# Kernel optimization log

Hardware: AMD Instinct MI355X
Metric: run time of the kernel (lower is better)

Reference implementation:

```python
import jax, jax.numpy as jnp
import numpy as np

A = 81          # agents / zones (9x9 grid)
DMAX = 5        # max neighborhood size (self + 4-neighbors)
NGLOB = 48      # global obs block width
HID = 128
B = 16384
LN_EPS = 1e-12  # tf.contrib.layers.layer_norm epsilon
BN_EPS = 1e-3   # tf.contrib.layers.batch_norm epsilon
NEG = -1e30


def _grid_adjacency():
    side = 9
    idx = np.zeros((A, DMAX), np.int32)
    mask = np.zeros((A, DMAX), bool)
    for i in range(A):
        r, c = divmod(i, side)
        nb = [i]
        for dr, dc in ((-1, 0), (1, 0), (0, -1), (0, 1)):
            rr, cc = r + dr, c + dc
            if 0 <= rr < side and 0 <= cc < side:
                nb.append(rr * side + cc)
        idx[i, :len(nb)] = nb
        mask[i, :len(nb)] = True
    return jnp.asarray(idx), jnp.asarray(mask)


def setup_inputs() -> dict:
    key = jax.random.key(0)
    ks = jax.random.split(key, 8)
    neigh_idx, neigh_mask = _grid_adjacency()
    in_dim = 2 * DMAX + NGLOB  # padded local obs width (58)
    s = 0.05
    return {
        "obs": jax.random.normal(ks[0], (B, 210), jnp.float32),
        "neigh_idx": neigh_idx,
        "neigh_mask": neigh_mask,
        "W1": jax.random.normal(ks[1], (A, in_dim, HID), jnp.float32) * s,
        "b1": jnp.zeros((A, HID), jnp.float32),
        "ln1_g": jnp.ones((A, HID), jnp.float32),
        "ln1_b": jnp.zeros((A, HID), jnp.float32),
        "bn1_b": jnp.zeros((A, HID), jnp.float32),
        "W2": jax.random.normal(ks[2], (A, HID, HID), jnp.float32) * s,
        "b2": jnp.zeros((A, HID), jnp.float32),
        "ln2_g": jnp.ones((A, HID), jnp.float32),
        "ln2_b": jnp.zeros((A, HID), jnp.float32),
        "bn2_b": jnp.zeros((A, HID), jnp.float32),
        "Wout": jax.random.normal(ks[3], (A, HID, DMAX), jnp.float32) * s,
        "bout": jnp.zeros((A, DMAX), jnp.float32),
    }


def _layer_norm(x, g, b):
    mu = jnp.mean(x, axis=-1, keepdims=True)
    var = jnp.mean(jnp.square(x - mu), axis=-1, keepdims=True)
    return (x - mu) * jax.lax.rsqrt(var + LN_EPS) * g[:, None, :] + b[:, None, :]


def _batch_norm(x, beta):
    # training-mode batch norm over the batch axis (axis=1), center only (scale=False)
    mu = jnp.mean(x, axis=1, keepdims=True)
    var = jnp.mean(jnp.square(x - mu), axis=1, keepdims=True)
    return (x - mu) * jax.lax.rsqrt(var + BN_EPS) + beta[:, None, :]


def reference(obs, neigh_idx, neigh_mask, W1, b1, ln1_g, ln1_b, bn1_b,
              W2, b2, ln2_g, ln2_b, bn2_b, Wout, bout):
    m = neigh_mask[:, None, :].astype(obs.dtype)          # [A,1,DMAX]
    g1 = obs[:, NGLOB + neigh_idx].transpose(1, 0, 2)      # [A,B,DMAX] zone block 1
    g2 = obs[:, NGLOB + 81 + neigh_idx].transpose(1, 0, 2)  # [A,B,DMAX] zone block 2
    glob = jnp.broadcast_to(obs[None, :, :NGLOB], (A, obs.shape[0], NGLOB))
    x = jnp.concatenate([g1 * m, g2 * m, glob], axis=-1)   # [A,B,58] (padded slots zeroed)

    h = jnp.einsum('abi,aio->abo', x, W1) + b1[:, None, :]
    h = jax.nn.relu(_batch_norm(_layer_norm(h, ln1_g, ln1_b), bn1_b))
    h = jnp.einsum('abi,aio->abo', h, W2) + b2[:, None, :]
    h = jax.nn.relu(_batch_norm(_layer_norm(h, ln2_g, ln2_b), bn2_b))

    logits = jnp.einsum('abi,aid->abd', h, Wout) + bout[:, None, :]  # [A,B,DMAX]
    logits = jnp.where(neigh_mask[:, None, :], logits, NEG)
    p = jax.nn.softmax(logits, axis=-1) * m                # masked softmax over valid neighbors

    oh = jax.nn.one_hot(neigh_idx, A, dtype=p.dtype)       # [A,DMAX,81] scatter map
    out = jnp.einsum('abd,adn->abn', p, oh)                # scatter into fixed 81-vector
    return out.transpose(1, 0, 2)                          # [B,A,81]
```

## Files before the change

### kernel.cpp

```cpp
#include <hip/hip_runtime.h>
#include <stdint.h>
#include <stddef.h>

#define N_AG 81

typedef __bf16 bf16x8 __attribute__((ext_vector_type(8)));
typedef float f32x4 __attribute__((ext_vector_type(4)));
typedef uint32_t u32v4 __attribute__((ext_vector_type(4)));
typedef uint32_t u32v2 __attribute__((ext_vector_type(2)));

#define PB 0
#define PG 128
#define PBT 256

#define SWZ(row, off) ((uint32_t)(off) ^ (((uint32_t)(row) & 7u) << 4))

__device__ __forceinline__ unsigned short b2u(__bf16 h) {
  return __builtin_bit_cast(unsigned short, h);
}

__device__ __forceinline__ f32x4 f4z() { f32x4 v; v[0]=0.f; v[1]=0.f; v[2]=0.f; v[3]=0.f; return v; }

__device__ __forceinline__ bf16x8 ld_frag(const uint8_t* p) {
  u32v4 v = *(const u32v4*)p;
  return __builtin_bit_cast(bf16x8, v);
}

__device__ __forceinline__ f32x4 mfma16(bf16x8 a, bf16x8 b, f32x4 c) {
  return __builtin_amdgcn_mfma_f32_16x16x32_bf16(a, b, c, 0, 0, 0);
}

__device__ __forceinline__ uint8_t* yslot(float* out, int b, int a) {
  size_t base = (size_t)b * 26244 + (size_t)a * 324;
  uint32_t pad = (uint32_t)(64 - (base & 63)) & 63u;
  return (uint8_t*)out + base + pad;
}

__device__ __forceinline__ float wave16_sum(float v) {
  v += __builtin_bit_cast(float, __builtin_amdgcn_update_dpp(0, __builtin_bit_cast(int, v), 0xB1, 0xF, 0xF, true));
  v += __builtin_bit_cast(float, __builtin_amdgcn_update_dpp(0, __builtin_bit_cast(int, v), 0x4E, 0xF, 0xF, true));
  v += __builtin_bit_cast(float, __builtin_amdgcn_update_dpp(0, __builtin_bit_cast(int, v), 0x141, 0xF, 0xF, true));
  v += __builtin_bit_cast(float, __builtin_amdgcn_update_dpp(0, __builtin_bit_cast(int, v), 0x140, 0xF, 0xF, true));
  return v;
}

__device__ __forceinline__ bf16x8 mk_frag(const unsigned short (&us)[8]) {
  u32v4 pk;
  pk[0] = (uint32_t)us[0] | ((uint32_t)us[1] << 16);
  pk[1] = (uint32_t)us[2] | ((uint32_t)us[3] << 16);
  pk[2] = (uint32_t)us[4] | ((uint32_t)us[5] << 16);
  pk[3] = (uint32_t)us[6] | ((uint32_t)us[7] << 16);
  return __builtin_bit_cast(bf16x8, pk);
}

__device__ __forceinline__ bf16x8 bn_frag(u32v4 yv, const f32x4 (&cf)[4]) {
  bf16x8 r;
  #pragma unroll
  for (int j = 0; j < 8; ++j) {
    uint32_t us = (j & 1) ? (yv[j >> 1] >> 16) : (yv[j >> 1] & 0xffffu);
    float f = __builtin_bit_cast(float, us << 16);
    float h = fmaf(f, cf[j >> 1][(j & 1) * 2], cf[j >> 1][(j & 1) * 2 + 1]);
    r[j] = (__bf16)fmaxf(h, 0.f);
  }
  return r;
}

__device__ __forceinline__ void bias_ln(f32x4 (&acc)[8][2], const float* s_par, int g) {
  #pragma unroll
  for (int nf = 0; nf < 2; ++nf) {
    float s = 0.f, qs = 0.f;
    #pragma unroll
    for (int mf = 0; mf < 8; ++mf) {
      #pragma unroll
      for (int rg = 0; rg < 4; ++rg) {
        float tv = acc[mf][nf][rg] + s_par[PB + 16 * mf + 4 * g + rg];
        acc[mf][nf][rg] = tv;
        s += tv;
        qs = fmaf(tv, tv, qs);
      }
    }
    s += __shfl_xor(s, 16);  s += __shfl_xor(s, 32);
    qs += __shfl_xor(qs, 16); qs += __shfl_xor(qs, 32);
    float mu = s * (1.f / 128.f);
    float var = qs * (1.f / 128.f) - mu * mu;
    float rstd = rsqrtf(var + 1e-12f);
    #pragma unroll
    for (int mf = 0; mf < 8; ++mf) {
      #pragma unroll
      for (int rg = 0; rg < 4; ++rg) {
        int o = 16 * mf + 4 * g + rg;
        acc[mf][nf][rg] = (acc[mf][nf][rg] - mu) * rstd * s_par[PG + o] + s_par[PBT + o];
      }
    }
  }
}

__device__ __forceinline__ void stats_lds(const f32x4 (&acc)[8][2],
                                          float (&s_red)[2][4][128],
                                          int wv, int g, int q) {
  #pragma unroll
  for (int mf = 0; mf < 8; ++mf) {
    #pragma unroll
    for (int rg = 0; rg < 4; ++rg) {
      float a0v = acc[mf][0][rg], a1v = acc[mf][1][rg];
      float s = a0v + a1v;
      float qq = fmaf(a0v, a0v, a1v * a1v);
      s = wave16_sum(s);
      qq = wave16_sum(qq);
      if (q == 0) {
        int o = 16 * mf + 4 * g + rg;
        s_red[0][wv][o] += s;
        s_red[1][wv][o] += qq;
      }
    }
  }
}

__device__ __forceinline__ void pack_lds(const f32x4 (&acc)[8][2], uint8_t* s_y,
                                         int wv, int g, int q) {
  #pragma unroll
  for (int nf = 0; nf < 2; ++nf) {
    uint32_t row = 32 * wv + 16 * nf + q;
    #pragma unroll
    for (int mf = 0; mf < 8; ++mf) {
      u32v2 pk;
      pk[0] = (uint32_t)b2u((__bf16)acc[mf][nf][0]) | ((uint32_t)b2u((__bf16)acc[mf][nf][1]) << 16);
      pk[1] = (uint32_t)b2u((__bf16)acc[mf][nf][2]) | ((uint32_t)b2u((__bf16)acc[mf][nf][3]) << 16);
      *(u32v2*)(s_y + row * 256 + SWZ(row, 32 * mf + 8 * g)) = pk;
    }
  }
}

__device__ __forceinline__ void burst_out(const uint8_t* s_y, float* out, int tile, int a, int t) {
  const int row = t >> 1, half = t & 1;
  uint8_t* sp = yslot(out, tile * 128 + row, a) + half * 128;
  #pragma unroll
  for (int j = 0; j < 8; ++j) {
    u32v4 v = *(const u32v4*)(s_y + row * 256 + SWZ(row, half * 128 + 16 * j));
    *(u32v4*)(sp + 16 * j) = v;
  }
}

__device__ __forceinline__ void burst_in(uint8_t* s_y, float* out, int tile, int a, int t) {
  const int row = t >> 1, half = t & 1;
  const uint8_t* sp = yslot(out, tile * 128 + row, a) + half * 128;
  #pragma unroll
  for (int j = 0; j < 8; ++j) {
    u32v4 v = *(const u32v4*)(sp + 16 * j);
    *(u32v4*)(s_y + row * 256 + SWZ(row, half * 128 + 16 * j)) = v;
  }
}

__global__ void prep_w1(const float* __restrict__ W1, uint8_t* __restrict__ w1img) {
  const int a = blockIdx.x, t = threadIdx.x;
  for (int i = t; i < 128 * 64; i += 256) {
    int o = i & 127, kk = i >> 7;
    float v;
    if (kk < 48)      v = W1[((size_t)a * 58 + (10 + kk)) * 128 + o];
    else if (kk < 58) v = W1[((size_t)a * 58 + (kk - 48)) * 128 + o];
    else              v = 0.f;
    uint32_t cb = 2u * kk;
    uint32_t phys = o * 128 + (((cb & ~15u) ^ (((uint32_t)o & 7u) << 4)) | (cb & 15u));
    *(unsigned short*)(w1img + (size_t)a * 16384 + phys) = b2u((__bf16)v);
  }
}

__global__ void prep_w2wo(const float* __restrict__ W2, const float* __restrict__ Wout,
                          uint8_t* __restrict__ w2img, uint8_t* __restrict__ woimg) {
  const int a = blockIdx.x, t = threadIdx.x;
  for (int i = t; i < 128 * 128; i += 256) {
    int o = i & 127, kk = i >> 7;
    float v = W2[((size_t)a * 128 + kk) * 128 + o];
    uint32_t cb = 2u * kk;
    uint32_t phys = o * 256 + (((cb & ~15u) ^ (((uint32_t)o & 7u) << 4)) | (cb & 15u));
    *(unsigned short*)(w2img + (size_t)a * 32768 + phys) = b2u((__bf16)v);
  }
  for (int i = t; i < 16 * 128; i += 256) {
    int k = i & 127, d = i >> 7;
    float v = (d < 5) ? Wout[((size_t)a * 128 + k) * 5 + d] : 0.f;
    uint32_t cb = 2u * k;
    uint32_t phys = d * 256 + (((cb & ~15u) ^ (((uint32_t)d & 7u) << 4)) | (cb & 15u));
    *(unsigned short*)(woimg + (size_t)a * 4096 + phys) = b2u((__bf16)v);
  }
}

__global__ void prep_obs(const float* __restrict__ obs, uint8_t* __restrict__ globimg) {
  const int row = blockIdx.x * 256 + threadIdx.x;
  if (row >= 16384) return;
  const float* orow = obs + (size_t)row * 210;
  uint8_t* dst = globimg + (size_t)row * 96;
  #pragma unroll
  for (int c = 0; c < 6; ++c) {
    u32v4 pk;
    #pragma unroll
    for (int e = 0; e < 4; ++e) {
      pk[e] = (uint32_t)b2u((__bf16)orow[8 * c + 2 * e]) |
              ((uint32_t)b2u((__bf16)orow[8 * c + 2 * e + 1]) << 16);
    }
    *(u32v4*)(dst + 16 * c) = pk;
  }
}

__global__ void prep_zimgT(const float* __restrict__ obs, unsigned short* __restrict__ zimgT) {
  __shared__ unsigned short lt[128][164];
  const int t = threadIdx.x;
  const int b0 = blockIdx.x * 128;
  for (int i = t; i < 128 * 162; i += 256) {
    int br = i / 162, n = i - 162 * br;
    lt[br][n] = b2u((__bf16)obs[(size_t)(b0 + br) * 210 + 48 + n]);
  }
  __syncthreads();
  for (int i = t; i < 162 * 128; i += 256) {
    int n = i >> 7, br = i & 127;
    zimgT[(size_t)n * 16384 + b0 + br] = lt[br][n];
  }
}

__global__ void reduce_bn(const float* __restrict__ S, const float* __restrict__ Q,
                          const float* __restrict__ beta, float2* __restrict__ bn) {
  const int a = blockIdx.x, k = threadIdx.x;
  float mu = S[a * 128 + k] * (1.f / 16384.f);
  float var = Q[a * 128 + k] * (1.f / 16384.f) - mu * mu;
  float rs = rsqrtf(var + 1e-3f);
  bn[a * 128 + k] = make_float2(rs, beta[a * 128 + k] - mu * rs);
}

__launch_bounds__(256, 2)
__global__ void pass1_kernel(const int* __restrict__ nidx,
                             const float* __restrict__ b1, const float* __restrict__ ln1g,
                             const float* __restrict__ ln1b,
                             const uint8_t* __restrict__ w1img,
                             const uint8_t* __restrict__ globimg,
                             const unsigned short* __restrict__ zimgT,
                             float* __restrict__ statS, float* __restrict__ statQ,
                             float* __restrict__ out) {
  __shared__ __align__(16) uint8_t s_w1[16384];
  __shared__ __align__(16) uint8_t s_y[32768];
  __shared__ float s_par[384];
  __shared__ float s_red[2][4][128];

  const int t = threadIdx.x;
  const int wv = t >> 6, l = t & 63, g = l >> 4, q = l & 15;
  const int a = blockIdx.x >> 5;
  const int sub = blockIdx.x & 31;

  const int r9 = a / 9, c9 = a - 9 * r9;
  const int deg = 1 + (r9 > 0) + (r9 < 8) + (c9 > 0) + (c9 < 8);
  int nid[5];
  #pragma unroll
  for (int d = 0; d < 5; ++d) nid[d] = __builtin_amdgcn_readfirstlane(nidx[a * 5 + d]);

  const uint8_t* w1src = w1img + (size_t)a * 16384;
  #pragma unroll
  for (int i = 0; i < 4; ++i) ((u32v4*)s_w1)[t + 256 * i] = ((const u32v4*)w1src)[t + 256 * i];
  if (t < 128) {
    s_par[PB + t] = b1[a * 128 + t];
    s_par[PG + t] = ln1g[a * 128 + t];
    s_par[PBT + t] = ln1b[a * 128 + t];
  }
  #pragma unroll
  for (int i = 0; i < 4; ++i) ((float*)s_red)[t + 256 * i] = 0.f;
  __syncthreads();

  for (int tt = 0; tt < 4; ++tt) {
    const int tile = sub * 4 + tt;

    bf16x8 bfr[2][2];
    #pragma unroll
    for (int ks = 0; ks < 2; ++ks) {
      #pragma unroll
      for (int nf = 0; nf < 2; ++nf) {
        const int brow = tile * 128 + 32 * wv + 16 * nf + q;
        if (ks == 1 && g >= 2) {
          unsigned short us[8];
          if (g == 2) {
            #pragma unroll
            for (int e = 0; e < 5; ++e)
              us[e] = (e < deg) ? zimgT[(size_t)nid[e] * 16384 + brow] : (unsigned short)0;
            #pragma unroll
            for (int e = 0; e < 3; ++e)
              us[5 + e] = (e < deg) ? zimgT[(size_t)(81 + nid[e]) * 16384 + brow] : (unsigned short)0;
          } else {
            us[0] = (3 < deg) ? zimgT[(size_t)(81 + nid[3]) * 16384 + brow] : (unsigned short)0;
            us[1] = (4 < deg) ? zimgT[(size_t)(81 + nid[4]) * 16384 + brow] : (unsigned short)0;
            #pragma unroll
            for (int e = 2; e < 8; ++e) us[e] = 0;
          }
          bfr[ks][nf] = mk_frag(us);
        } else {
          bfr[ks][nf] = *(const bf16x8*)(globimg + (size_t)brow * 96 + (32 * ks + 8 * g) * 2);
        }
      }
    }

    f32x4 acc[8][2];
    #pragma unroll
    for (int mf = 0; mf < 8; ++mf) { acc[mf][0] = f4z(); acc[mf][1] = f4z(); }
    #pragma unroll
    for (int ks = 0; ks < 2; ++ks) {
      #pragma unroll
      for (int mf = 0; mf < 8; ++mf) {
        uint32_t r = 16 * mf + q;
        uint32_t cb = ((uint32_t)(64 * ks + 16 * g)) ^ ((r & 7u) << 4);
        bf16x8 af = ld_frag(s_w1 + r * 128 + cb);
        acc[mf][0] = mfma16(af, bfr[ks][0], acc[mf][0]);
        acc[mf][1] = mfma16(af, bfr[ks][1], acc[mf][1]);
      }
    }

    bias_ln(acc, s_par, g);
    stats_lds(acc, s_red, wv, g, q);
    pack_lds(acc, s_y, wv, g, q);
    __syncthreads();
    burst_out(s_y, out, tile, a, t);
    __syncthreads();
  }

  if (t < 128) {
    float S = s_red[0][0][t] + s_red[0][1][t] + s_red[0][2][t] + s_red[0][3][t];
    float Q = s_red[1][0][t] + s_red[1][1][t] + s_red[1][2][t] + s_red[1][3][t];
    atomicAdd(statS + a * 128 + t, S);
    atomicAdd(statQ + a * 128 + t, Q);
  }
}

__launch_bounds__(256, 2)
__global__ void pass2_kernel(const float* __restrict__ b2, const float* __restrict__ ln2g,
                             const float* __restrict__ ln2b,
                             const uint8_t* __restrict__ w2img,
                             const float2* __restrict__ bn1,
                             float* __restrict__ statS, float* __restrict__ statQ,
                             float* __restrict__ out) {
  __shared__ __align__(16) uint8_t s_w2[32768];
  __shared__ __align__(16) uint8_t s_y[32768];
  __shared__ float s_par[384];
  __shared__ __align__(16) float2 s_bnc[128];
  __shared__ float s_red[2][4][128];

  const int t = threadIdx.x;
  const int wv = t >> 6, l = t & 63, g = l >> 4, q = l & 15;
  const int a = blockIdx.x >> 5;
  const int sub = blockIdx.x & 31;

  const uint8_t* w2src = w2img + (size_t)a * 32768;
  #pragma unroll
  for (int i = 0; i < 8; ++i) ((u32v4*)s_w2)[t + 256 * i] = ((const u32v4*)w2src)[t + 256 * i];
  if (t < 128) {
    s_par[PB + t] = b2[a * 128 + t];
    s_par[PG + t] = ln2g[a * 128 + t];
    s_par[PBT + t] = ln2b[a * 128 + t];
    s_bnc[t] = bn1[a * 128 + t];
  }
  #pragma unroll
  for (int i = 0; i < 4; ++i) ((float*)s_red)[t + 256 * i] = 0.f;
  __syncthreads();

  for (int tt = 0; tt < 4; ++tt) {
    const int tile = sub * 4 + tt;

    burst_in(s_y, out, tile, a, t);
    __syncthreads();

    f32x4 acc[8][2];
    #pragma unroll
    for (int mf = 0; mf < 8; ++mf) { acc[mf][0] = f4z(); acc[mf][1] = f4z(); }

    #pragma unroll
    for (int ks2 = 0; ks2 < 4; ++ks2) {
      const int k0 = 32 * ks2 + 8 * g;
      f32x4 cf[4];
      #pragma unroll
      for (int i = 0; i < 4; ++i)
        cf[i] = *(const f32x4*)((const uint8_t*)s_bnc + k0 * 8 + 16 * i);
      bf16x8 bfr[2];
      #pragma unroll
      for (int nf = 0; nf < 2; ++nf) {
        uint32_t row = 32 * wv + 16 * nf + q;
        u32v4 yv = *(const u32v4*)(s_y + row * 256 + SWZ(row, 64 * ks2 + 16 * g));
        bfr[nf] = bn_frag(yv, cf);
      }
      #pragma unroll
      for (int mf = 0; mf < 8; ++mf) {
        uint32_t r = 16 * mf + q;
        uint32_t cb = ((uint32_t)(64 * ks2 + 16 * g)) ^ ((r & 7u) << 4);
        bf16x8 af = ld_frag(s_w2 + r * 256 + cb);
        acc[mf][0] = mfma16(af, bfr[0], acc[mf][0]);
        acc[mf][1] = mfma16(af, bfr[1], acc[mf][1]);
      }
    }

    bias_ln(acc, s_par, g);
    stats_lds(acc, s_red, wv, g, q);
    __syncthreads();
    pack_lds(acc, s_y, wv, g, q);
    __syncthreads();
    burst_out(s_y, out, tile, a, t);
    __syncthreads();
  }

  if (t < 128) {
    float S = s_red[0][0][t] + s_red[0][1][t] + s_red[0][2][t] + s_red[0][3][t];
    float Q = s_red[1][0][t] + s_red[1][1][t] + s_red[1][2][t] + s_red[1][3][t];
    atomicAdd(statS + a * 128 + t, S);
    atomicAdd(statQ + a * 128 + t, Q);
  }
}

__launch_bounds__(256, 3)
__global__ void pass3_kernel(const int* __restrict__ nidx, const float* __restrict__ boutp,
                             const uint8_t* __restrict__ woimg,
                             const float2* __restrict__ bn2,
                             float* __restrict__ out) {
  __shared__ __align__(16) uint8_t s_buf[43008];
  __shared__ __align__(16) uint8_t s_wo[4096];
  __shared__ __align__(16) float2 s_bnc[128];
  __shared__ float s_bout[16];

  uint8_t* s_y = s_buf;
  float* s_out = (float*)s_buf;

  const int t = threadIdx.x;
  const int wv = t >> 6, l = t & 63, g = l >> 4, q = l & 15;
  const int a = blockIdx.x >> 5;
  const int sub = blockIdx.x & 31;

  const int r9 = a / 9, c9 = a - 9 * r9;
  const int deg = 1 + (r9 > 0) + (r9 < 8) + (c9 > 0) + (c9 < 8);
  int nid[5];
  #pragma unroll
  for (int d = 0; d < 5; ++d) nid[d] = __builtin_amdgcn_readfirstlane(nidx[a * 5 + d]);

  ((u32v4*)s_wo)[t] = ((const u32v4*)(woimg + (size_t)a * 4096))[t];
  if (t < 128) s_bnc[t] = bn2[a * 128 + t];
  if (t < 16) s_bout[t] = (t < 5) ? boutp[a * 5 + t] : 0.f;
  __syncthreads();

  bf16x8 afr[4];
  #pragma unroll
  for (int ks2 = 0; ks2 < 4; ++ks2) {
    uint32_t cb = ((uint32_t)(64 * ks2 + 16 * g)) ^ (((uint32_t)q & 7u) << 4);
    afr[ks2] = ld_frag(s_wo + q * 256 + cb);
  }

  for (int tt = 0; tt < 4; ++tt) {
    const int tile = sub * 4 + tt;

    burst_in(s_y, out, tile, a, t);
    __syncthreads();

    f32x4 accd[2];
    accd[0] = f4z(); accd[1] = f4z();

    #pragma unroll
    for (int ks2 = 0; ks2 < 4; ++ks2) {
      const int k0 = 32 * ks2 + 8 * g;
      f32x4 cf[4];
      #pragma unroll
      for (int i = 0; i < 4; ++i)
        cf[i] = *(const f32x4*)((const uint8_t*)s_bnc + k0 * 8 + 16 * i);
      #pragma unroll
      for (int nf = 0; nf < 2; ++nf) {
        uint32_t row = 32 * wv + 16 * nf + q;
        u32v4 yv = *(const u32v4*)(s_y + row * 256 + SWZ(row, 64 * ks2 + 16 * g));
        accd[nf] = mfma16(afr[ks2], bn_frag(yv, cf), accd[nf]);
      }
    }

    #pragma unroll
    for (int nf = 0; nf < 2; ++nf) {
      #pragma unroll
      for (int rg = 0; rg < 4; ++rg) accd[nf][rg] += s_bout[4 * g + rg];
    }
    float d4[2];
    d4[0] = __shfl_xor(accd[0][0], 16);
    d4[1] = __shfl_xor(accd[1][0], 16);

    float p[2][5];
    #pragma unroll
    for (int nf = 0; nf < 2; ++nf) {
      float v[5] = {accd[nf][0], accd[nf][1], accd[nf][2], accd[nf][3], d4[nf]};
      float mx = v[0];
      #pragma unroll
      for (int d = 1; d < 5; ++d)
        if (d < deg) mx = fmaxf(mx, v[d]);
      float den = 0.f;
      #pragma unroll
      for (int d = 0; d < 5; ++d) {
        float e = (d < deg) ? __expf(v[d] - mx) : 0.f;
        p[nf][d] = e;
        den += e;
      }
      float inv = 1.f / den;
      #pragma unroll
      for (int d = 0; d < 5; ++d) p[nf][d] *= inv;
    }

    float p5[5];
    #pragma unroll
    for (int d = 0; d < 5; ++d) {
      float pr = __shfl_xor(p[1][d], 32);
      p5[d] = (g == 0) ? p[0][d] : pr;
    }

    __syncthreads();
    #pragma unroll
    for (int i = 0; i < 11; ++i) {
      int idx = t + 256 * i;
      if (idx < 2688) {
        u32v4 z; z[0] = 0u; z[1] = 0u; z[2] = 0u; z[3] = 0u;
        ((u32v4*)s_out)[idx] = z;
      }
    }
    __syncthreads();
    if (g == 0 || g == 2) {
      const int row = 32 * wv + ((g == 2) ? 16 : 0) + q;
      #pragma unroll
      for (int d = 0; d < 5; ++d)
        if (d < deg) s_out[row * 84 + nid[d]] = p5[d];
    }
    __syncthreads();
    const size_t obase = (size_t)(tile * 128) * 6561 + (size_t)a * 81;
    for (int i = t; i < 128 * 81; i += 256) {
      int r = i / 81;
      int n = i - r * 81;
      out[obase + (size_t)r * 6561 + n] = s_out[r * 84 + n];
    }
    __syncthreads();
  }
}

extern "C" void kernel_launch(void* const* d_in, const int* in_sizes, int n_in,
                              void* d_out, int out_size, void* d_ws, size_t ws_size,
                              hipStream_t stream) {
  (void)in_sizes; (void)n_in; (void)out_size; (void)ws_size;
  const float* obs = (const float*)d_in[0];
  const int* nidx = (const int*)d_in[1];
  const float* W1 = (const float*)d_in[3];
  const float* b1 = (const float*)d_in[4];
  const float* ln1g = (const float*)d_in[5];
  const float* ln1b = (const float*)d_in[6];
  const float* bnb1 = (const float*)d_in[7];
  const float* W2 = (const float*)d_in[8];
  const float* b2 = (const float*)d_in[9];
  const float* ln2g = (const float*)d_in[10];
  const float* ln2b = (const float*)d_in[11];
  const float* bnb2 = (const float*)d_in[12];
  const float* Wout = (const float*)d_in[13];
  const float* bout = (const float*)d_in[14];
  float* out = (float*)d_out;
  uint8_t* ws = (uint8_t*)d_ws;

  uint8_t* w1img   = ws;
  uint8_t* globimg = ws + 1327104;
  uint8_t* regionA = ws + 2899968;
  unsigned short* zimgT = (unsigned short*)regionA;
  uint8_t* w2img = regionA;
  uint8_t* woimg = regionA + 2654208;
  float* statS = (float*)(ws + 8208384);
  float* statQ = (float*)(ws + 8249856);
  float2* bn1 = (float2*)(ws + 8291328);
  float2* bn2 = (float2*)(ws + 8374272);

  prep_w1<<<N_AG, 256, 0, stream>>>(W1, w1img);
  prep_obs<<<64, 256, 0, stream>>>(obs, globimg);
  prep_zimgT<<<128, 256, 0, stream>>>(obs, zimgT);
  hipMemsetAsync(statS, 0, 2 * 41472, stream);

  pass1_kernel<<<N_AG * 32, 256, 0, stream>>>(nidx, b1, ln1g, ln1b, w1img, globimg, zimgT,
                                              statS, statQ, out);
  reduce_bn<<<N_AG, 128, 0, stream>>>(statS, statQ, bnb1, bn1);

  prep_w2wo<<<N_AG, 256, 0, stream>>>(W2, Wout, w2img, woimg);
  hipMemsetAsync(statS, 0, 2 * 41472, stream);

  pass2_kernel<<<N_AG * 32, 256, 0, stream>>>(b2, ln2g, ln2b, w2img, bn1,
                                              statS, statQ, out);
  reduce_bn<<<N_AG, 128, 0, stream>>>(statS, statQ, bnb2, bn2);

  pass3_kernel<<<N_AG * 32, 256, 0, stream>>>(nidx, bout, woimg, bn2, out);
}
```

Measured before the change: 777.8 us.

## Recompute hidden layers per pass instead of spilling activations through output buffer

Instead of writing the layer-1 and layer-2 activations to the output buffer as scratch and reading them back in later passes, each pass now recomputes earlier layers from obs: pass2 redoes GEMM1 and pass3 redoes GEMM1 and GEMM2. The zone-transpose prep kernel is removed, and zone features are gathered directly from obs. Weights are read from global memory instead of being staged in LDS, which lowers LDS use and allows higher occupancy bounds. This trades a large amount of intermediate global traffic for extra MFMA work and scattered obs reads.

```diff
diff --git a/kernel.cpp b/kernel.cpp
--- a/kernel.cpp
+++ b/kernel.cpp
@@ -13,7 +13,7 @@
 #define PG 128
 #define PBT 256
 
-#define SWZ(row, off) ((uint32_t)(off) ^ (((uint32_t)(row) & 7u) << 4))
+#define SWZ(row, off) ((uint32_t)(off) ^ (((uint32_t)(row) & 15u) << 4))
 
 __device__ __forceinline__ unsigned short b2u(__bf16 h) {
   return __builtin_bit_cast(unsigned short, h);
@@ -28,12 +28,6 @@
 
 __device__ __forceinline__ f32x4 mfma16(bf16x8 a, bf16x8 b, f32x4 c) {
   return __builtin_amdgcn_mfma_f32_16x16x32_bf16(a, b, c, 0, 0, 0);
-}
-
-__device__ __forceinline__ uint8_t* yslot(float* out, int b, int a) {
-  size_t base = (size_t)b * 26244 + (size_t)a * 324;
-  uint32_t pad = (uint32_t)(64 - (base & 63)) & 63u;
-  return (uint8_t*)out + base + pad;
 }
 
 __device__ __forceinline__ float wave16_sum(float v) {
@@ -53,16 +47,79 @@
   return __builtin_bit_cast(bf16x8, pk);
 }
 
-__device__ __forceinline__ bf16x8 bn_frag(u32v4 yv, const f32x4 (&cf)[4]) {
-  bf16x8 r;
-  #pragma unroll
-  for (int j = 0; j < 8; ++j) {
-    uint32_t us = (j & 1) ? (yv[j >> 1] >> 16) : (yv[j >> 1] & 0xffffu);
-    float f = __builtin_bit_cast(float, us << 16);
-    float h = fmaf(f, cf[j >> 1][(j & 1) * 2], cf[j >> 1][(j & 1) * 2 + 1]);
-    r[j] = (__bf16)fmaxf(h, 0.f);
-  }
-  return r;
+__device__ __forceinline__ bf16x8 zone_frag(const float* orow, const int (&nid)[5],
+                                            int deg, int g) {
+  unsigned short us[8];
+  if (g == 2) {
+    #pragma unroll
+    for (int e = 0; e < 8; ++e) {
+      float v;
+      if (e < 5) v = (e < deg) ? orow[48 + nid[e]] : 0.f;
+      else       v = ((e - 5) < deg) ? orow[129 + nid[e - 5]] : 0.f;
+      us[e] = b2u((__bf16)v);
+    }
+  } else {
+    us[0] = (3 < deg) ? b2u((__bf16)orow[129 + nid[3]]) : (unsigned short)0;
+    us[1] = (4 < deg) ? b2u((__bf16)orow[129 + nid[4]]) : (unsigned short)0;
+    #pragma unroll
+    for (int e = 2; e < 8; ++e) us[e] = 0;
+  }
+  return mk_frag(us);
+}
+
+__device__ __forceinline__ void build_xfrags(bf16x8 (&bfr)[2][2],
+                                             const uint8_t* __restrict__ globimg,
+                                             const float* __restrict__ obs,
+                                             int tile, int wv, int g, int q,
+                                             const int (&nid)[5], int deg) {
+  #pragma unroll
+  for (int ks = 0; ks < 2; ++ks) {
+    #pragma unroll
+    for (int nf = 0; nf < 2; ++nf) {
+      const int brow = tile * 128 + 32 * wv + 16 * nf + q;
+      if (ks == 1 && g >= 2) {
+        bfr[ks][nf] = zone_frag(obs + (size_t)brow * 210, nid, deg, g);
+      } else {
+        bfr[ks][nf] = *(const bf16x8*)(globimg + (size_t)brow * 96 + (32 * ks + 8 * g) * 2);
+      }
+    }
+  }
+}
+
+__device__ __forceinline__ void gemm1(f32x4 (&acc)[8][2], const bf16x8 (&bfr)[2][2],
+                                      const uint8_t* __restrict__ w1a, int g, int q) {
+  #pragma unroll
+  for (int ks = 0; ks < 2; ++ks) {
+    #pragma unroll
+    for (int mf = 0; mf < 8; ++mf) {
+      uint32_t r = 16 * mf + q;
+      uint32_t cb = ((uint32_t)(64 * ks + 16 * g)) ^ ((r & 7u) << 4);
+      bf16x8 af = ld_frag(w1a + r * 128 + cb);
+      acc[mf][0] = mfma16(af, bfr[ks][0], acc[mf][0]);
+      acc[mf][1] = mfma16(af, bfr[ks][1], acc[mf][1]);
+    }
+  }
+}
+
+__device__ __forceinline__ void gemm2(f32x4 (&acc)[8][2], const uint8_t* __restrict__ s_y,
+                                      const uint8_t* __restrict__ w2a, int wv, int g, int q) {
+  #pragma unroll
+  for (int ks2 = 0; ks2 < 4; ++ks2) {
+    bf16x8 bfr2[2];
+    #pragma unroll
+    for (int nf = 0; nf < 2; ++nf) {
+      uint32_t row = 32 * wv + 16 * nf + q;
+      bfr2[nf] = ld_frag(s_y + row * 256 + SWZ(row, 64 * ks2 + 16 * g));
+    }
+    #pragma unroll
+    for (int mf = 0; mf < 8; ++mf) {
+      uint32_t r = 16 * mf + q;
+      uint32_t cb = ((uint32_t)(64 * ks2 + 16 * g)) ^ ((r & 7u) << 4);
+      bf16x8 af = ld_frag(w2a + r * 256 + cb);
+      acc[mf][0] = mfma16(af, bfr2[0], acc[mf][0]);
+      acc[mf][1] = mfma16(af, bfr2[1], acc[mf][1]);
+    }
+  }
 }
 
 __device__ __forceinline__ void bias_ln(f32x4 (&acc)[8][2], const float* s_par, int g) {
@@ -116,38 +173,26 @@
   }
 }
 
-__device__ __forceinline__ void pack_lds(const f32x4 (&acc)[8][2], uint8_t* s_y,
-                                         int wv, int g, int q) {
+__device__ __forceinline__ void pack_h(const f32x4 (&acc)[8][2], const float2* s_bnc,
+                                       uint8_t* s_y, int wv, int g, int q) {
   #pragma unroll
   for (int nf = 0; nf < 2; ++nf) {
     uint32_t row = 32 * wv + 16 * nf + q;
     #pragma unroll
     for (int mf = 0; mf < 8; ++mf) {
+      unsigned short us[4];
+      #pragma unroll
+      for (int rg = 0; rg < 4; ++rg) {
+        int o = 16 * mf + 4 * g + rg;
+        float2 c = s_bnc[o];
+        float h = fmaf(acc[mf][nf][rg], c.x, c.y);
+        us[rg] = b2u((__bf16)fmaxf(h, 0.f));
+      }
       u32v2 pk;
-      pk[0] = (uint32_t)b2u((__bf16)acc[mf][nf][0]) | ((uint32_t)b2u((__bf16)acc[mf][nf][1]) << 16);
-      pk[1] = (uint32_t)b2u((__bf16)acc[mf][nf][2]) | ((uint32_t)b2u((__bf16)acc[mf][nf][3]) << 16);
+      pk[0] = (uint32_t)us[0] | ((uint32_t)us[1] << 16);
+      pk[1] = (uint32_t)us[2] | ((uint32_t)us[3] << 16);
       *(u32v2*)(s_y + row * 256 + SWZ(row, 32 * mf + 8 * g)) = pk;
     }
-  }
-}
-
-__device__ __forceinline__ void burst_out(const uint8_t* s_y, float* out, int tile, int a, int t) {
-  const int row = t >> 1, half = t & 1;
-  uint8_t* sp = yslot(out, tile * 128 + row, a) + half * 128;
-  #pragma unroll
-  for (int j = 0; j < 8; ++j) {
-    u32v4 v = *(const u32v4*)(s_y + row * 256 + SWZ(row, half * 128 + 16 * j));
-    *(u32v4*)(sp + 16 * j) = v;
-  }
-}
-
-__device__ __forceinline__ void burst_in(uint8_t* s_y, float* out, int tile, int a, int t) {
-  const int row = t >> 1, half = t & 1;
-  const uint8_t* sp = yslot(out, tile * 128 + row, a) + half * 128;
-  #pragma unroll
-  for (int j = 0; j < 8; ++j) {
-    u32v4 v = *(const u32v4*)(sp + 16 * j);
-    *(u32v4*)(s_y + row * 256 + SWZ(row, half * 128 + 16 * j)) = v;
   }
 }
 
@@ -201,21 +246,6 @@
   }
 }
 
-__global__ void prep_zimgT(const float* __restrict__ obs, unsigned short* __restrict__ zimgT) {
-  __shared__ unsigned short lt[128][164];
-  const int t = threadIdx.x;
-  const int b0 = blockIdx.x * 128;
-  for (int i = t; i < 128 * 162; i += 256) {
-    int br = i / 162, n = i - 162 * br;
-    lt[br][n] = b2u((__bf16)obs[(size_t)(b0 + br) * 210 + 48 + n]);
-  }
-  __syncthreads();
-  for (int i = t; i < 162 * 128; i += 256) {
-    int n = i >> 7, br = i & 127;
-    zimgT[(size_t)n * 16384 + b0 + br] = lt[br][n];
-  }
-}
-
 __global__ void reduce_bn(const float* __restrict__ S, const float* __restrict__ Q,
                           const float* __restrict__ beta, float2* __restrict__ bn) {
   const int a = blockIdx.x, k = threadIdx.x;
@@ -225,18 +255,14 @@
   bn[a * 128 + k] = make_float2(rs, beta[a * 128 + k] - mu * rs);
 }
 
-__launch_bounds__(256, 2)
-__global__ void pass1_kernel(const int* __restrict__ nidx,
+__launch_bounds__(256, 4)
+__global__ void pass1_kernel(const float* __restrict__ obs, const int* __restrict__ nidx,
                              const float* __restrict__ b1, const float* __restrict__ ln1g,
                              const float* __restrict__ ln1b,
                              const uint8_t* __restrict__ w1img,
                              const uint8_t* __restrict__ globimg,
-                             const unsigned short* __restrict__ zimgT,
-                             float* __restrict__ statS, float* __restrict__ statQ,
-                             float* __restrict__ out) {
-  __shared__ __align__(16) uint8_t s_w1[16384];
-  __shared__ __align__(16) uint8_t s_y[32768];
-  __shared__ float s_par[384];
+                             float* __restrict__ statS, float* __restrict__ statQ) {
+  __shared__ float s_parA[384];
   __shared__ float s_red[2][4][128];
 
   const int t = threadIdx.x;
@@ -250,72 +276,30 @@
   #pragma unroll
   for (int d = 0; d < 5; ++d) nid[d] = __builtin_amdgcn_readfirstlane(nidx[a * 5 + d]);
 
-  const uint8_t* w1src = w1img + (size_t)a * 16384;
-  #pragma unroll
-  for (int i = 0; i < 4; ++i) ((u32v4*)s_w1)[t + 256 * i] = ((const u32v4*)w1src)[t + 256 * i];
   if (t < 128) {
-    s_par[PB + t] = b1[a * 128 + t];
-    s_par[PG + t] = ln1g[a * 128 + t];
-    s_par[PBT + t] = ln1b[a * 128 + t];
+    s_parA[PB + t] = b1[a * 128 + t];
+    s_parA[PG + t] = ln1g[a * 128 + t];
+    s_parA[PBT + t] = ln1b[a * 128 + t];
   }
   #pragma unroll
   for (int i = 0; i < 4; ++i) ((float*)s_red)[t + 256 * i] = 0.f;
   __syncthreads();
 
+  const uint8_t* w1a = w1img + (size_t)a * 16384;
+
   for (int tt = 0; tt < 4; ++tt) {
     const int tile = sub * 4 + tt;
-
     bf16x8 bfr[2][2];
-    #pragma unroll
-    for (int ks = 0; ks < 2; ++ks) {
-      #pragma unroll
-      for (int nf = 0; nf < 2; ++nf) {
-        const int brow = tile * 128 + 32 * wv + 16 * nf + q;
-        if (ks == 1 && g >= 2) {
-          unsigned short us[8];
-          if (g == 2) {
-            #pragma unroll
-            for (int e = 0; e < 5; ++e)
-              us[e] = (e < deg) ? zimgT[(size_t)nid[e] * 16384 + brow] : (unsigned short)0;
-            #pragma unroll
-            for (int e = 0; e < 3; ++e)
-              us[5 + e] = (e < deg) ? zimgT[(size_t)(81 + nid[e]) * 16384 + brow] : (unsigned short)0;
-          } else {
-            us[0] = (3 < deg) ? zimgT[(size_t)(81 + nid[3]) * 16384 + brow] : (unsigned short)0;
-            us[1] = (4 < deg) ? zimgT[(size_t)(81 + nid[4]) * 16384 + brow] : (unsigned short)0;
-            #pragma unroll
-            for (int e = 2; e < 8; ++e) us[e] = 0;
-          }
-          bfr[ks][nf] = mk_frag(us);
-        } else {
-          bfr[ks][nf] = *(const bf16x8*)(globimg + (size_t)brow * 96 + (32 * ks + 8 * g) * 2);
-        }
-      }
-    }
-
+    build_xfrags(bfr, globimg, obs, tile, wv, g, q, nid, deg);
     f32x4 acc[8][2];
     #pragma unroll
     for (int mf = 0; mf < 8; ++mf) { acc[mf][0] = f4z(); acc[mf][1] = f4z(); }
-    #pragma unroll
-    for (int ks = 0; ks < 2; ++ks) {
-      #pragma unroll
-      for (int mf = 0; mf < 8; ++mf) {
-        uint32_t r = 16 * mf + q;
-        uint32_t cb = ((uint32_t)(64 * ks + 16 * g)) ^ ((r & 7u) << 4);
-        bf16x8 af = ld_frag(s_w1 + r * 128 + cb);
-        acc[mf][0] = mfma16(af, bfr[ks][0], acc[mf][0]);
-        acc[mf][1] = mfma16(af, bfr[ks][1], acc[mf][1]);
-      }
-    }
-
-    bias_ln(acc, s_par, g);
+    gemm1(acc, bfr, w1a, g, q);
+    bias_ln(acc, s_parA, g);
     stats_lds(acc, s_red, wv, g, q);
-    pack_lds(acc, s_y, wv, g, q);
-    __syncthreads();
-    burst_out(s_y, out, tile, a, t);
-    __syncthreads();
-  }
-
+  }
+
+  __syncthreads();
   if (t < 128) {
     float S = s_red[0][0][t] + s_red[0][1][t] + s_red[0][2][t] + s_red[0][3][t];
     float Q = s_red[1][0][t] + s_red[1][1][t] + s_red[1][2][t] + s_red[1][3][t];
@@ -324,17 +308,21 @@
   }
 }
 
-__launch_bounds__(256, 2)
-__global__ void pass2_kernel(const float* __restrict__ b2, const float* __restrict__ ln2g,
+__launch_bounds__(256, 3)
+__global__ void pass2_kernel(const float* __restrict__ obs, const int* __restrict__ nidx,
+                             const float* __restrict__ b1, const float* __restrict__ ln1g,
+                             const float* __restrict__ ln1b,
+                             const float* __restrict__ b2, const float* __restrict__ ln2g,
                              const float* __restrict__ ln2b,
+                             const uint8_t* __restrict__ w1img,
                              const uint8_t* __restrict__ w2img,
+                             const uint8_t* __restrict__ globimg,
                              const float2* __restrict__ bn1,
-                             float* __restrict__ statS, float* __restrict__ statQ,
-                             float* __restrict__ out) {
-  __shared__ __align__(16) uint8_t s_w2[32768];
+                             float* __restrict__ statS, float* __restrict__ statQ) {
   __shared__ __align__(16) uint8_t s_y[32768];
-  __shared__ float s_par[384];
-  __shared__ __align__(16) float2 s_bnc[128];
+  __shared__ float s_parA[384];
+  __shared__ float s_parB[384];
+  __shared__ __align__(16) float2 s_bnc1[128];
   __shared__ float s_red[2][4][128];
 
   const int t = threadIdx.x;
@@ -342,62 +330,51 @@
   const int a = blockIdx.x >> 5;
   const int sub = blockIdx.x & 31;
 
-  const uint8_t* w2src = w2img + (size_t)a * 32768;
-  #pragma unroll
-  for (int i = 0; i < 8; ++i) ((u32v4*)s_w2)[t + 256 * i] = ((const u32v4*)w2src)[t + 256 * i];
+  const int r9 = a / 9, c9 = a - 9 * r9;
+  const int deg = 1 + (r9 > 0) + (r9 < 8) + (c9 > 0) + (c9 < 8);
+  int nid[5];
+  #pragma unroll
+  for (int d = 0; d < 5; ++d) nid[d] = __builtin_amdgcn_readfirstlane(nidx[a * 5 + d]);
+
   if (t < 128) {
-    s_par[PB + t] = b2[a * 128 + t];
-    s_par[PG + t] = ln2g[a * 128 + t];
-    s_par[PBT + t] = ln2b[a * 128 + t];
-    s_bnc[t] = bn1[a * 128 + t];
+    s_parA[PB + t] = b1[a * 128 + t];
+    s_parA[PG + t] = ln1g[a * 128 + t];
+    s_parA[PBT + t] = ln1b[a * 128 + t];
+    s_parB[PB + t] = b2[a * 128 + t];
+    s_parB[PG + t] = ln2g[a * 128 + t];
+    s_parB[PBT + t] = ln2b[a * 128 + t];
+    s_bnc1[t] = bn1[a * 128 + t];
   }
   #pragma unroll
   for (int i = 0; i < 4; ++i) ((float*)s_red)[t + 256 * i] = 0.f;
   __syncthreads();
 
+  const uint8_t* w1a = w1img + (size_t)a * 16384;
+  const uint8_t* w2a = w2img + (size_t)a * 32768;
+
   for (int tt = 0; tt < 4; ++tt) {
     const int tile = sub * 4 + tt;
-
-    burst_in(s_y, out, tile, a, t);
-    __syncthreads();
-
-    f32x4 acc[8][2];
-    #pragma unroll
-    for (int mf = 0; mf < 8; ++mf) { acc[mf][0] = f4z(); acc[mf][1] = f4z(); }
-
-    #pragma unroll
-    for (int ks2 = 0; ks2 < 4; ++ks2) {
-      const int k0 = 32 * ks2 + 8 * g;
-      f32x4 cf[4];
-      #pragma unroll
-      for (int i = 0; i < 4; ++i)
-        cf[i] = *(const f32x4*)((const uint8_t*)s_bnc + k0 * 8 + 16 * i);
-      bf16x8 bfr[2];
-      #pragma unroll
-      for (int nf = 0; nf < 2; ++nf) {
-        uint32_t row = 32 * wv + 16 * nf + q;
-        u32v4 yv = *(const u32v4*)(s_y + row * 256 + SWZ(row, 64 * ks2 + 16 * g));
-        bfr[nf] = bn_frag(yv, cf);
-      }
-      #pragma unroll
-      for (int mf = 0; mf < 8; ++mf) {
-        uint32_t r = 16 * mf + q;
-        uint32_t cb = ((uint32_t)(64 * ks2 + 16 * g)) ^ ((r & 7u) << 4);
-        bf16x8 af = ld_frag(s_w2 + r * 256 + cb);
-        acc[mf][0] = mfma16(af, bfr[0], acc[mf][0]);
-        acc[mf][1] = mfma16(af, bfr[1], acc[mf][1]);
-      }
-    }
-
-    bias_ln(acc, s_par, g);
-    stats_lds(acc, s_red, wv, g, q);
-    __syncthreads();
-    pack_lds(acc, s_y, wv, g, q);
-    __syncthreads();
-    burst_out(s_y, out, tile, a, t);
-    __syncthreads();
-  }
-
+    bf16x8 bfr[2][2];
+    build_xfrags(bfr, globimg, obs, tile, wv, g, q, nid, deg);
+    f32x4 acc1[8][2];
+    #pragma unroll
+    for (int mf = 0; mf < 8; ++mf) { acc1[mf][0] = f4z(); acc1[mf][1] = f4z(); }
+    gemm1(acc1, bfr, w1a, g, q);
+    bias_ln(acc1, s_parA, g);
+
+    __syncthreads();
+    pack_h(acc1, s_bnc1, s_y, wv, g, q);
+    __syncthreads();
+
+    f32x4 acc2[8][2];
+    #pragma unroll
+    for (int mf = 0; mf < 8; ++mf) { acc2[mf][0] = f4z(); acc2[mf][1] = f4z(); }
+    gemm2(acc2, s_y, w2a, wv, g, q);
+    bias_ln(acc2, s_parB, g);
+    stats_lds(acc2, s_red, wv, g, q);
+  }
+
+  __syncthreads();
   if (t < 128) {
     float S = s_red[0][0][t] + s_red[0][1][t] + s_red[0][2][t] + s_red[0][3][t];
     float Q = s_red[1][0][t] + s_red[1][1][t] + s_red[1][2][t] + s_red[1][3][t];
@@ -407,13 +384,23 @@
 }
 
 __launch_bounds__(256, 3)
-__global__ void pass3_kernel(const int* __restrict__ nidx, const float* __restrict__ boutp,
+__global__ void pass3_kernel(const float* __restrict__ obs, const int* __restrict__ nidx,
+                             const float* __restrict__ b1, const float* __restrict__ ln1g,
+                             const float* __restrict__ ln1b,
+                             const float* __restrict__ b2, const float* __restrict__ ln2g,
+                             const float* __restrict__ ln2b,
+                             const float* __restrict__ boutp,
+                             const uint8_t* __restrict__ w1img,
+                             const uint8_t* __restrict__ w2img,
                              const uint8_t* __restrict__ woimg,
-                             const float2* __restrict__ bn2,
+                             const uint8_t* __restrict__ globimg,
+                             const float2* __restrict__ bn1, const float2* __restrict__ bn2,
                              float* __restrict__ out) {
   __shared__ __align__(16) uint8_t s_buf[43008];
-  __shared__ __align__(16) uint8_t s_wo[4096];
-  __shared__ __align__(16) float2 s_bnc[128];
+  __shared__ float s_parA[384];
+  __shared__ float s_parB[384];
+  __shared__ __align__(16) float2 s_bnc1[128];
+  __shared__ __align__(16) float2 s_bnc2[128];
   __shared__ float s_bout[16];
 
   uint8_t* s_y = s_buf;
@@ -430,39 +417,64 @@
   #pragma unroll
   for (int d = 0; d < 5; ++d) nid[d] = __builtin_amdgcn_readfirstlane(nidx[a * 5 + d]);
 
-  ((u32v4*)s_wo)[t] = ((const u32v4*)(woimg + (size_t)a * 4096))[t];
-  if (t < 128) s_bnc[t] = bn2[a * 128 + t];
+  if (t < 128) {
+    s_parA[PB + t] = b1[a * 128 + t];
+    s_parA[PG + t] = ln1g[a * 128 + t];
+    s_parA[PBT + t] = ln1b[a * 128 + t];
+    s_parB[PB + t] = b2[a * 128 + t];
+    s_parB[PG + t] = ln2g[a * 128 + t];
+    s_parB[PBT + t] = ln2b[a * 128 + t];
+    s_bnc1[t] = bn1[a * 128 + t];
+    s_bnc2[t] = bn2[a * 128 + t];
+  }
   if (t < 16) s_bout[t] = (t < 5) ? boutp[a * 5 + t] : 0.f;
   __syncthreads();
 
+  const uint8_t* w1a = w1img + (size_t)a * 16384;
+  const uint8_t* w2a = w2img + (size_t)a * 32768;
+  const uint8_t* woa = woimg + (size_t)a * 4096;
+
   bf16x8 afr[4];
   #pragma unroll
   for (int ks2 = 0; ks2 < 4; ++ks2) {
     uint32_t cb = ((uint32_t)(64 * ks2 + 16 * g)) ^ (((uint32_t)q & 7u) << 4);
-    afr[ks2] = ld_frag(s_wo + q * 256 + cb);
+    afr[ks2] = ld_frag(woa + q * 256 + cb);
   }
 
   for (int tt = 0; tt < 4; ++tt) {
     const int tile = sub * 4 + tt;
 
-    burst_in(s_y, out, tile, a, t);
+    bf16x8 bfr[2][2];
+    build_xfrags(bfr, globimg, obs, tile, wv, g, q, nid, deg);
+    f32x4 acc1[8][2];
+    #pragma unroll
+    for (int mf = 0; mf < 8; ++mf) { acc1[mf][0] = f4z(); acc1[mf][1] = f4z(); }
+    gemm1(acc1, bfr, w1a, g, q);
+    bias_ln(acc1, s_parA, g);
+
+    __syncthreads();
+    pack_h(acc1, s_bnc1, s_y, wv, g, q);
+    __syncthreads();
+
+    f32x4 acc2[8][2];
+    #pragma unroll
+    for (int mf = 0; mf < 8; ++mf) { acc2[mf][0] = f4z(); acc2[mf][1] = f4z(); }
+    gemm2(acc2, s_y, w2a, wv, g, q);
+    bias_ln(acc2, s_parB, g);
+
+    __syncthreads();
+    pack_h(acc2, s_bnc2, s_y, wv, g, q);
     __syncthreads();
 
     f32x4 accd[2];
     accd[0] = f4z(); accd[1] = f4z();
-
     #pragma unroll
     for (int ks2 = 0; ks2 < 4; ++ks2) {
-      const int k0 = 32 * ks2 + 8 * g;
-      f32x4 cf[4];
-      #pragma unroll
-      for (int i = 0; i < 4; ++i)
-        cf[i] = *(const f32x4*)((const uint8_t*)s_bnc + k0 * 8 + 16 * i);
       #pragma unroll
       for (int nf = 0; nf < 2; ++nf) {
         uint32_t row = 32 * wv + 16 * nf + q;
-        u32v4 yv = *(const u32v4*)(s_y + row * 256 + SWZ(row, 64 * ks2 + 16 * g));
-        accd[nf] = mfma16(afr[ks2], bn_frag(yv, cf), accd[nf]);
+        bf16x8 hb = ld_frag(s_y + row * 256 + SWZ(row, 64 * ks2 + 16 * g));
+        accd[nf] = mfma16(afr[ks2], hb, accd[nf]);
       }
     }
 
@@ -525,7 +537,6 @@
       int n = i - r * 81;
       out[obase + (size_t)r * 6561 + n] = s_out[r * 84 + n];
     }
-    __syncthreads();
   }
 }
 
@@ -552,30 +563,29 @@
 
   uint8_t* w1img   = ws;
   uint8_t* globimg = ws + 1327104;
-  uint8_t* regionA = ws + 2899968;
-  unsigned short* zimgT = (unsigned short*)regionA;
-  uint8_t* w2img = regionA;
-  uint8_t* woimg = regionA + 2654208;
-  float* statS = (float*)(ws + 8208384);
-  float* statQ = (float*)(ws + 8249856);
-  float2* bn1 = (float2*)(ws + 8291328);
-  float2* bn2 = (float2*)(ws + 8374272);
+  uint8_t* w2img   = ws + 2899968;
+  uint8_t* woimg   = ws + 5554176;
+  float* statS1 = (float*)(ws + 5885952);
+  float* statQ1 = (float*)(ws + 5927424);
+  float* statS2 = (float*)(ws + 5968896);
+  float* statQ2 = (float*)(ws + 6010368);
+  float2* bn1 = (float2*)(ws + 6051840);
+  float2* bn2 = (float2*)(ws + 6134784);
 
   prep_w1<<<N_AG, 256, 0, stream>>>(W1, w1img);
+  prep_w2wo<<<N_AG, 256, 0, stream>>>(W2, Wout, w2img, woimg);
   prep_obs<<<64, 256, 0, stream>>>(obs, globimg);
-  prep_zimgT<<<128, 256, 0, stream>>>(obs, zimgT);
-  hipMemsetAsync(statS, 0, 2 * 41472, stream);
-
-  pass1_kernel<<<N_AG * 32, 256, 0, stream>>>(nidx, b1, ln1g, ln1b, w1img, globimg, zimgT,
-                                              statS, statQ, out);
-  reduce_bn<<<N_AG, 128, 0, stream>>>(statS, statQ, bnb1, bn1);
-
-  prep_w2wo<<<N_AG, 256, 0, stream>>>(W2, Wout, w2img, woimg);
-  hipMemsetAsync(statS, 0, 2 * 41472, stream);
-
-  pass2_kernel<<<N_AG * 32, 256, 0, stream>>>(b2, ln2g, ln2b, w2img, bn1,
-                                              statS, statQ, out);
-  reduce_bn<<<N_AG, 128, 0, stream>>>(statS, statQ, bnb2, bn2);
-
-  pass3_kernel<<<N_AG * 32, 256, 0, stream>>>(nidx, bout, woimg, bn2, out);
-}
+  hipMemsetAsync(statS1, 0, 4 * 41472, stream);
+
+  pass1_kernel<<<N_AG * 32, 256, 0, stream>>>(obs, nidx, b1, ln1g, ln1b, w1img, globimg,
+                                              statS1, statQ1);
+  reduce_bn<<<N_AG, 128, 0, stream>>>(statS1, statQ1, bnb1, bn1);
+
+  pass2_kernel<<<N_AG * 32, 256, 0, stream>>>(obs, nidx, b1, ln1g, ln1b, b2, ln2g, ln2b,
+                                              w1img, w2img, globimg, bn1, statS2, statQ2);
+  reduce_bn<<<N_AG, 128, 0, stream>>>(statS2, statQ2, bnb2, bn2);
+
+  pass3_kernel<<<N_AG * 32, 256, 0, stream>>>(obs, nidx, b1, ln1g, ln1b, b2, ln2g, ln2b,
+                                              bout, w1img, w2img, woimg, globimg,
+                                              bn1, bn2, out);
+}
```

After: 2.262 ms. +190.8%, slower.

## Make tile stages wave-local, drop block barriers, and prefetch next tile into registers

Applied to the files above, without the earlier changes.

The kernels rely on each wave reading and writing only its own 32 rows of the LDS staging buffer and its own slice of the statistics buffer. That lets most per-tile __syncthreads calls in pass1 and pass2 be removed. Pass2 and pass3 now load the next tile's activations from global memory into registers while the current tile is being computed, so global load latency overlaps with MFMA work. Pass3's output scatter, which zeroes the buffer, places the probabilities and writes out, is now done per wave over its own rows, removing two block barriers. The risk is correctness: any hidden cross-wave LDS dependency would become a race, and holding the prefetched tile adds register pressure.

```diff
diff --git a/kernel.cpp b/kernel.cpp
--- a/kernel.cpp
+++ b/kernel.cpp
@@ -141,14 +141,18 @@
   }
 }
 
-__device__ __forceinline__ void burst_in(uint8_t* s_y, float* out, int tile, int a, int t) {
+__device__ __forceinline__ void load_yregs(u32v4 (&yr)[8], const float* out, int tile, int a, int t) {
   const int row = t >> 1, half = t & 1;
-  const uint8_t* sp = yslot(out, tile * 128 + row, a) + half * 128;
-  #pragma unroll
-  for (int j = 0; j < 8; ++j) {
-    u32v4 v = *(const u32v4*)(sp + 16 * j);
-    *(u32v4*)(s_y + row * 256 + SWZ(row, half * 128 + 16 * j)) = v;
-  }
+  const uint8_t* sp = yslot((float*)out, tile * 128 + row, a) + half * 128;
+  #pragma unroll
+  for (int j = 0; j < 8; ++j) yr[j] = *(const u32v4*)(sp + 16 * j);
+}
+
+__device__ __forceinline__ void write_yregs(uint8_t* s_y, const u32v4 (&yr)[8], int t) {
+  const int row = t >> 1, half = t & 1;
+  #pragma unroll
+  for (int j = 0; j < 8; ++j)
+    *(u32v4*)(s_y + row * 256 + SWZ(row, half * 128 + 16 * j)) = yr[j];
 }
 
 __global__ void prep_w1(const float* __restrict__ W1, uint8_t* __restrict__ w1img) {
@@ -311,11 +315,10 @@
     bias_ln(acc, s_par, g);
     stats_lds(acc, s_red, wv, g, q);
     pack_lds(acc, s_y, wv, g, q);
-    __syncthreads();
     burst_out(s_y, out, tile, a, t);
-    __syncthreads();
-  }
-
+  }
+
+  __syncthreads();
   if (t < 128) {
     float S = s_red[0][0][t] + s_red[0][1][t] + s_red[0][2][t] + s_red[0][3][t];
     float Q = s_red[1][0][t] + s_red[1][1][t] + s_red[1][2][t] + s_red[1][3][t];
@@ -353,13 +356,16 @@
   }
   #pragma unroll
   for (int i = 0; i < 4; ++i) ((float*)s_red)[t + 256 * i] = 0.f;
+
+  u32v4 yreg[8];
+  load_yregs(yreg, out, sub * 4, a, t);
   __syncthreads();
 
   for (int tt = 0; tt < 4; ++tt) {
     const int tile = sub * 4 + tt;
 
-    burst_in(s_y, out, tile, a, t);
-    __syncthreads();
+    write_yregs(s_y, yreg, t);
+    if (tt < 3) load_yregs(yreg, out, tile + 1, a, t);
 
     f32x4 acc[8][2];
     #pragma unroll
@@ -391,13 +397,11 @@
 
     bias_ln(acc, s_par, g);
     stats_lds(acc, s_red, wv, g, q);
-    __syncthreads();
     pack_lds(acc, s_y, wv, g, q);
-    __syncthreads();
     burst_out(s_y, out, tile, a, t);
-    __syncthreads();
-  }
-
+  }
+
+  __syncthreads();
   if (t < 128) {
     float S = s_red[0][0][t] + s_red[0][1][t] + s_red[0][2][t] + s_red[0][3][t];
     float Q = s_red[1][0][t] + s_red[1][1][t] + s_red[1][2][t] + s_red[1][3][t];
@@ -433,6 +437,9 @@
   ((u32v4*)s_wo)[t] = ((const u32v4*)(woimg + (size_t)a * 4096))[t];
   if (t < 128) s_bnc[t] = bn2[a * 128 + t];
   if (t < 16) s_bout[t] = (t < 5) ? boutp[a * 5 + t] : 0.f;
+
+  u32v4 yreg[8];
+  load_yregs(yreg, out, sub * 4, a, t);
   __syncthreads();
 
   bf16x8 afr[4];
@@ -445,8 +452,8 @@
   for (int tt = 0; tt < 4; ++tt) {
     const int tile = sub * 4 + tt;
 
-    burst_in(s_y, out, tile, a, t);
-    __syncthreads();
+    write_yregs(s_y, yreg, t);
+    if (tt < 3) load_yregs(yreg, out, tile + 1, a, t);
 
     f32x4 accd[2];
     accd[0] = f4z(); accd[1] = f4z();
@@ -503,28 +510,28 @@
     }
 
     __syncthreads();
-    #pragma unroll
-    for (int i = 0; i < 11; ++i) {
-      int idx = t + 256 * i;
-      if (idx < 2688) {
+
+    {
+      const uint32_t fbase = 84u * 32u * wv;
+      for (int i = l; i < 672; i += 64) {
         u32v4 z; z[0] = 0u; z[1] = 0u; z[2] = 0u; z[3] = 0u;
-        ((u32v4*)s_out)[idx] = z;
-      }
-    }
-    __syncthreads();
-    if (g == 0 || g == 2) {
-      const int row = 32 * wv + ((g == 2) ? 16 : 0) + q;
-      #pragma unroll
-      for (int d = 0; d < 5; ++d)
-        if (d < deg) s_out[row * 84 + nid[d]] = p5[d];
-    }
-    __syncthreads();
-    const size_t obase = (size_t)(tile * 128) * 6561 + (size_t)a * 81;
-    for (int i = t; i < 128 * 81; i += 256) {
-      int r = i / 81;
-      int n = i - r * 81;
-      out[obase + (size_t)r * 6561 + n] = s_out[r * 84 + n];
-    }
+        *(u32v4*)((uint8_t*)s_out + (size_t)fbase * 4 + (size_t)i * 16) = z;
+      }
+      if (g == 0 || g == 2) {
+        const int row = 32 * wv + ((g == 2) ? 16 : 0) + q;
+        #pragma unroll
+        for (int d = 0; d < 5; ++d)
+          if (d < deg) s_out[row * 84 + nid[d]] = p5[d];
+      }
+      const size_t obase = (size_t)(tile * 128) * 6561 + (size_t)a * 81;
+      for (int i = l; i < 32 * 81; i += 64) {
+        int rr = i / 81;
+        int n = i - rr * 81;
+        int row = 32 * wv + rr;
+        out[obase + (size_t)row * 6561 + n] = s_out[row * 84 + n];
+      }
+    }
+
     __syncthreads();
   }
 }
```

Result: slower. 934.9 us (+20.2%).
